# Performance work log

Hardware: AMD Instinct MI355X
Metric: run time of the kernel (lower is better)

## Reference

```python
import jax, jax.numpy as jnp
import numpy as np

NUM_HEADS = 16
ROPE_THETA = 10000.0
SCALE_FACTOR = 1.0  # max_position_embeddings / block_size


def _rope_cos_sin(T, head_dim, dtype):
    # standard RoPE frequencies: inv_freq_i = theta^(-2i/d)
    inv_freq = 1.0 / (ROPE_THETA ** (jnp.arange(0, head_dim, 2, dtype=jnp.float32) / head_dim))
    pos = jnp.arange(T, dtype=jnp.float32) / SCALE_FACTOR
    ang = pos[:, None] * inv_freq[None, :]            # (T, D/2)
    ang = jnp.concatenate([ang, ang], axis=-1)        # (T, D)
    return jnp.cos(ang).astype(dtype)[None, None], jnp.sin(ang).astype(dtype)[None, None]


def _rotate_half(u):
    d = u.shape[-1] // 2
    return jnp.concatenate([-u[..., d:], u[..., :d]], axis=-1)


def setup_inputs() -> dict:
    key = jax.random.key(0)
    ks = jax.random.split(key, 5)
    B, T, C = 2, 2048, 1024
    x = jax.random.normal(ks[0], (B, T, C), dtype=jnp.float32)
    Wqkv = jax.random.normal(ks[1], (C, 3 * C), dtype=jnp.float32) * (1.0 / np.sqrt(C))
    bqkv = jnp.zeros((3 * C,), dtype=jnp.float32)
    Wproj = jax.random.normal(ks[2], (C, C), dtype=jnp.float32) * (1.0 / np.sqrt(C))
    bproj = jnp.zeros((C,), dtype=jnp.float32)
    return {"x": x, "Wqkv": Wqkv, "bqkv": bqkv, "Wproj": Wproj, "bproj": bproj}


def reference(x, Wqkv, bqkv, Wproj, bproj):
    B, T, C = x.shape
    H = NUM_HEADS
    D = C // H
    qkv = x @ Wqkv + bqkv                              # (B, T, 3C)
    q, k, v = jnp.split(qkv, 3, axis=-1)
    # (B, H, T, D)
    q = q.reshape(B, T, H, D).transpose(0, 2, 1, 3)
    k = k.reshape(B, T, H, D).transpose(0, 2, 1, 3)
    v = v.reshape(B, T, H, D).transpose(0, 2, 1, 3)
    cos, sin = _rope_cos_sin(T, D, x.dtype)
    q = q * cos + _rotate_half(q) * sin
    k = k * cos + _rotate_half(k) * sin
    att = jnp.einsum('bhtd,bhsd->bhts', q, k) / jnp.sqrt(jnp.asarray(D, x.dtype))
    causal = jnp.tril(jnp.ones((T, T), dtype=bool))
    att = jnp.where(causal[None, None], att, jnp.asarray(-jnp.inf, att.dtype))
    att = jax.nn.softmax(att, axis=-1)
    y = jnp.einsum('bhts,bhsd->bhtd', att, v)          # (B, H, T, D)
    y = y.transpose(0, 2, 1, 3).reshape(B, T, C)
    return y @ Wproj + bproj
```

## Files before the change

### kernel.cpp

```cpp
#include <hip/hip_runtime.h>
#include <hip/hip_bf16.h>

typedef __hip_bfloat16 bf16;
typedef __attribute__((ext_vector_type(8))) __bf16 bf16x8;
typedef __attribute__((ext_vector_type(4))) __bf16 bf16x4;
typedef __attribute__((ext_vector_type(4))) float f32x4;
typedef unsigned short u16;

#define MFMA16(a, b, c) __builtin_amdgcn_mfma_f32_16x16x32_bf16((a), (b), (c), 0, 0, 0)

static constexpr int B_ = 2, T_ = 2048, C_ = 1024, H_ = 16, D_ = 64;
static constexpr int BT = B_ * T_;
static constexpr int N3 = 3 * C_;

__device__ __forceinline__ void gload16(void* lds, const void* g) {
    __builtin_amdgcn_global_load_lds(
        (const __attribute__((address_space(1))) unsigned int*)g,
        (__attribute__((address_space(3))) unsigned int*)lds, 16, 0, 0);
}

__device__ __forceinline__ u16 bb(float x) {
    return __builtin_bit_cast(u16, __float2bfloat16(x));
}


__global__ void k_transpose_w(const float* __restrict__ src, bf16* __restrict__ dst,
                              int K, int N) {
    __shared__ float t[32][33];
    int bx = blockIdx.x * 32;
    int by = blockIdx.y * 32;
    int tx = threadIdx.x & 31, ty = threadIdx.x >> 5;
#pragma unroll
    for (int i = 0; i < 32; i += 8)
        t[ty + i][tx] = src[(size_t)(by + ty + i) * N + bx + tx];
    __syncthreads();
#pragma unroll
    for (int i = 0; i < 32; i += 8)
        dst[(size_t)(bx + ty + i) * K + by + tx] = __float2bfloat16(t[tx][ty + i]);
}

__global__ void k_convert_x(const float* __restrict__ src, bf16* __restrict__ dst, int n4) {
    int i = blockIdx.x * 256 + threadIdx.x;
    if (i >= n4) return;
    float4 v = reinterpret_cast<const float4*>(src)[i];
    dst[4 * i + 0] = __float2bfloat16(v.x);
    dst[4 * i + 1] = __float2bfloat16(v.y);
    dst[4 * i + 2] = __float2bfloat16(v.z);
    dst[4 * i + 3] = __float2bfloat16(v.w);
}

__global__ void k_rope_table(float* __restrict__ ct, float* __restrict__ st) {
    int i = blockIdx.x * 256 + threadIdx.x;
    if (i >= T_ * 32) return;
    int t = i >> 5, f = i & 31;
    float invf = exp2f(-(float)f * 0.4152410118609203f);
    float ang = (float)t * invf;
    ct[i] = cosf(ang);
    st[i] = sinf(ang);
}

__global__ __launch_bounds__(256) void k_gemm_qkv(
    const bf16* __restrict__ A, const bf16* __restrict__ Bt,
    const float* __restrict__ bias,
    const float* __restrict__ ct, const float* __restrict__ st,
    bf16* __restrict__ q, bf16* __restrict__ kk, bf16* __restrict__ vt) {
    __shared__ bf16 lA[2][128 * 32];
    __shared__ bf16 lB[2][128 * 32];
    const int tid = threadIdx.x;
    const int wave = tid >> 6, lane = tid & 63;
    const int wm = wave >> 1, wn = wave & 1;
    const int l16 = lane & 15, lg = lane >> 4;
    const int m0 = blockIdx.y * 128, n0 = blockIdx.x * 128;

    f32x4 acc[4][4];
#pragma unroll
    for (int i = 0; i < 4; i++)
#pragma unroll
        for (int j = 0; j < 4; j++) acc[i][j] = (f32x4){0.f, 0.f, 0.f, 0.f};

    const int r = lane >> 2;
    const int sc = (lane & 3) ^ (r & 3);
    const bf16* gA = A + (size_t)(m0 + wave * 32 + r) * 1024 + sc * 8;
    const bf16* gB = Bt + (size_t)(n0 + wave * 32 + r) * 1024 + sc * 8;
    const int sw = (lg ^ (l16 & 3)) * 8;

    auto stage = [&](int buf, int k0) {
        bf16* sA = lA[buf] + wave * 1024;
        bf16* sB = lB[buf] + wave * 1024;
        gload16(sA, gA + k0);
        gload16(sA + 512, gA + (size_t)16 * 1024 + k0);
        gload16(sB, gB + k0);
        gload16(sB + 512, gB + (size_t)16 * 1024 + k0);
    };

    stage(0, 0);
    int buf = 0;
    for (int k0 = 0; k0 < 1024; k0 += 32) {
        __syncthreads();
        if (k0 + 32 < 1024) stage(buf ^ 1, k0 + 32);
        bf16x8 af[4], bfr[4];
#pragma unroll
        for (int mi = 0; mi < 4; mi++)
            af[mi] = *(const bf16x8*)(lA[buf] + (wm * 64 + mi * 16 + l16) * 32 + sw);
#pragma unroll
        for (int nj = 0; nj < 4; nj++)
            bfr[nj] = *(const bf16x8*)(lB[buf] + (wn * 64 + nj * 16 + l16) * 32 + sw);
#pragma unroll
        for (int mi = 0; mi < 4; mi++)
#pragma unroll
            for (int nj = 0; nj < 4; nj++)
                acc[mi][nj] = MFMA16(af[mi], bfr[nj], acc[mi][nj]);
        buf ^= 1;
    }

    const int b = m0 >> 11;
#pragma unroll
    for (int mi = 0; mi < 4; mi++) {
        int mbase = m0 + wm * 64 + mi * 16 + lg * 4;
#pragma unroll
        for (int nj = 0; nj < 4; nj++) {
            int n = n0 + wn * 64 + nj * 16 + l16;
            int which = n >> 10;
            int nq = n & 1023;
            int h = nq >> 6, d = nq & 63;
#pragma unroll
            for (int rr = 0; rr < 4; rr++) {
                int m = mbase + rr;
                int t = m & 2047;
                float v = acc[mi][nj][rr] + bias[n];
                if (which == 2) {
                    vt[((size_t)(b * 16 + h) * 64 + d) * 2048 + t] = __float2bfloat16(v);
                } else {
                    float pv = acc[mi][nj ^ 2][rr] + bias[n ^ 32];
                    float c = ct[t * 32 + (d & 31)];
                    float s = st[t * 32 + (d & 31)];
                    float rh = (d < 32) ? -pv : pv;
                    float o = v * c + rh * s;
                    bf16* dst = (which == 0) ? q : kk;
                    dst[((size_t)(b * 16 + h) * 2048 + t) * 64 + d] = __float2bfloat16(o);
                }
            }
        }
    }
}

__global__ __launch_bounds__(256, 4) void k_attn(
    const bf16* __restrict__ qg, const bf16* __restrict__ kg,
    const bf16* __restrict__ vtg, bf16* __restrict__ y) {
    __shared__ bf16 smem[2][2][4096];
    const int wv = threadIdx.x >> 6;
    const int pair = wv >> 1, qh = wv & 1;
    const int lane = threadIdx.x & 63;
    const int l16 = lane & 15, lg = lane >> 4;
    const int id = blockIdx.x;
    const int bh = id & 31;
    const int s = 31 - (id >> 5);
    const int q0w = s * 64 + 32 * qh;
    const bf16* qh_p = qg + (size_t)bh * (2048 * 64);
    const bf16* kh = kg + (size_t)bh * (2048 * 64);
    const bf16* vh = vtg + (size_t)bh * (64 * 2048);

    bf16x8 qf[2][2];
#pragma unroll
    for (int g = 0; g < 2; g++)
#pragma unroll
        for (int h = 0; h < 2; h++)
            qf[g][h] = *(const bf16x8*)(qh_p + (size_t)(q0w + 16 * g + l16) * 64 + 32 * h + 8 * lg);

    f32x4 o[2][4];
#pragma unroll
    for (int g = 0; g < 2; g++)
#pragma unroll
        for (int dt = 0; dt < 4; dt++) o[g][dt] = (f32x4){0.f, 0.f, 0.f, 0.f};
    float mm[2] = {-1e30f, -1e30f}, ls[2] = {0.f, 0.f};

    auto stage = [&](int buf, int kt) {
        bf16* lk = &smem[pair][buf][0];
        bf16* lv = &smem[pair][buf][2048];
#pragma unroll
        for (int i = 0; i < 2; i++) {
            int cc = 2 * qh + i;
            {
                int row = 8 * cc + (lane >> 3);
                int scc = (lane & 7) ^ (lane >> 3);
                gload16(&lk[cc * 512], kh + (size_t)(kt + row) * 64 + scc * 8);
            }
            {
                int row = 16 * cc + (lane >> 2);
                int su = (lane & 3) ^ ((lane >> 3) & 3);
                gload16(&lv[cc * 512], vh + (size_t)row * 2048 + kt + su * 8);
            }
        }
    };

    const f32x4 z = (f32x4){0.f, 0.f, 0.f, 0.f};
    auto compute = [&](int buf, bool diag) {
        const bf16* lk = &smem[pair][buf][0];
        const bf16* lv = &smem[pair][buf][2048];
        bf16x8 kf2[2][2];
#pragma unroll
        for (int t = 0; t < 2; t++)
#pragma unroll
            for (int h = 0; h < 2; h++) {
                int krow = 16 * t + l16;
                int koff = ((h * 64 + lg * 16) ^ ((l16 & 7) << 4)) >> 1;
                kf2[t][h] = *(const bf16x8*)(&lk[krow * 64 + koff]);
            }
        bf16x8 vf[4];
#pragma unroll
        for (int dt = 0; dt < 4; dt++) {
            int vrow = 16 * dt + l16;
            int rs = (l16 >> 1) & 3;
            const bf16* vb = &lv[vrow * 32];
            bf16x4 lo = *(const bf16x4*)(vb + (((lg >> 1) ^ rs) * 8 + (lg & 1) * 4));
            bf16x4 hi = *(const bf16x4*)(vb + (((2 + (lg >> 1)) ^ rs) * 8 + (lg & 1) * 4));
            vf[dt] = __builtin_shufflevector(lo, hi, 0, 1, 2, 3, 4, 5, 6, 7);
        }
        f32x4 sg[2][2];
#pragma unroll
        for (int g = 0; g < 2; g++)
#pragma unroll
            for (int t = 0; t < 2; t++) {
                f32x4 acc = MFMA16(kf2[t][0], qf[g][0], z);
                sg[g][t] = MFMA16(kf2[t][1], qf[g][1], acc);
            }
#pragma unroll
        for (int g = 0; g < 2; g++) {
            float p[8];
#pragma unroll
            for (int t = 0; t < 2; t++)
#pragma unroll
                for (int rr = 0; rr < 4; rr++) {
                    float v = sg[g][t][rr] * 0.125f;
                    if (diag && (16 * t + 4 * lg + rr > 16 * g + l16)) v = -1e30f;
                    p[4 * t + rr] = v;
                }
            float pm = p[0];
#pragma unroll
            for (int i = 1; i < 8; i++) pm = fmaxf(pm, p[i]);
            pm = fmaxf(pm, __shfl_xor(pm, 16, 64));
            pm = fmaxf(pm, __shfl_xor(pm, 32, 64));
            float mn = fmaxf(mm[g], pm);
            float al = __expf(mm[g] - mn);
#pragma unroll
            for (int dt = 0; dt < 4; dt++) o[g][dt] *= al;
            ls[g] *= al;
            mm[g] = mn;
            float ps = 0.f;
#pragma unroll
            for (int i = 0; i < 8; i++) {
                p[i] = __expf(p[i] - mn);
                ps += p[i];
            }
            ls[g] += ps;
            bf16x8 pf;
#pragma unroll
            for (int j = 0; j < 8; j++)
                pf[j] = __builtin_bit_cast(__bf16, __float2bfloat16(p[j]));
#pragma unroll
            for (int dt = 0; dt < 4; dt++) o[g][dt] = MFMA16(vf[dt], pf, o[g][dt]);
        }
    };

    const int base = pair ? (s + 1) : 0;
    const int niter = s + 1;
    stage(0, 32 * base);
    for (int i = 0; i < niter; ++i) {
        __syncthreads();
        if (i + 1 < niter) stage((i + 1) & 1, 32 * (base + i + 1));
        int kt = 32 * (base + i);
        if (kt <= q0w) compute(i & 1, kt == q0w);
    }

    __syncthreads();
    float* mg = (float*)&smem[0][0][0];
    if (pair == 1) {
        float* pp = mg + (qh * 64 + lane) * 36;
        pp[0] = mm[0]; pp[1] = mm[1]; pp[2] = ls[0]; pp[3] = ls[1];
#pragma unroll
        for (int g = 0; g < 2; g++)
#pragma unroll
            for (int dt = 0; dt < 4; dt++)
#pragma unroll
                for (int rr = 0; rr < 4; rr++)
                    pp[4 + g * 16 + dt * 4 + rr] = o[g][dt][rr];
    }
    __syncthreads();
    if (pair == 0) {
        const float* pp = mg + (qh * 64 + lane) * 36;
#pragma unroll
        for (int g = 0; g < 2; g++) {
            float m1 = pp[g], l1 = pp[2 + g];
            float mn = fmaxf(mm[g], m1);
            float a0 = __expf(mm[g] - mn);
            float a1 = __expf(m1 - mn);
            ls[g] = ls[g] * a0 + l1 * a1;
#pragma unroll
            for (int dt = 0; dt < 4; dt++)
#pragma unroll
                for (int rr = 0; rr < 4; rr++)
                    o[g][dt][rr] = o[g][dt][rr] * a0 + pp[4 + g * 16 + dt * 4 + rr] * a1;
        }
        const int b = bh >> 4, h = bh & 15;
#pragma unroll
        for (int g = 0; g < 2; g++) {
            float lt = ls[g];
            lt += __shfl_xor(lt, 16, 64);
            lt += __shfl_xor(lt, 32, 64);
            float inv = 1.f / lt;
            bf16* yp = y + ((size_t)(b * 2048 + q0w + 16 * g + l16)) * 1024 + h * 64 + 4 * lg;
#pragma unroll
            for (int dt = 0; dt < 4; dt++) {
                *(ushort4*)(yp + 16 * dt) = make_ushort4(
                    bb(o[g][dt][0] * inv), bb(o[g][dt][1] * inv),
                    bb(o[g][dt][2] * inv), bb(o[g][dt][3] * inv));
            }
        }
    }
}

__global__ __launch_bounds__(256) void k_gemm_proj(
    const bf16* __restrict__ A, const bf16* __restrict__ Bt,
    const float* __restrict__ bias, float* __restrict__ out) {
    __shared__ bf16 lA[2][128 * 32];
    __shared__ bf16 lB[2][128 * 32];
    const int tid = threadIdx.x;
    const int wave = tid >> 6, lane = tid & 63;
    const int wm = wave >> 1, wn = wave & 1;
    const int l16 = lane & 15, lg = lane >> 4;
    const int m0 = blockIdx.y * 128, n0 = blockIdx.x * 128;

    f32x4 acc[4][4];
#pragma unroll
    for (int i = 0; i < 4; i++)
#pragma unroll
        for (int j = 0; j < 4; j++) acc[i][j] = (f32x4){0.f, 0.f, 0.f, 0.f};

    const int r = lane >> 2;
    const int sc = (lane & 3) ^ (r & 3);
    const bf16* gA = A + (size_t)(m0 + wave * 32 + r) * 1024 + sc * 8;
    const bf16* gB = Bt + (size_t)(n0 + wave * 32 + r) * 1024 + sc * 8;
    const int sw = (lg ^ (l16 & 3)) * 8;

    auto stage = [&](int buf, int k0) {
        bf16* sA = lA[buf] + wave * 1024;
        bf16* sB = lB[buf] + wave * 1024;
        gload16(sA, gA + k0);
        gload16(sA + 512, gA + (size_t)16 * 1024 + k0);
        gload16(sB, gB + k0);
        gload16(sB + 512, gB + (size_t)16 * 1024 + k0);
    };

    stage(0, 0);
    int buf = 0;
    for (int k0 = 0; k0 < 1024; k0 += 32) {
        __syncthreads();
        if (k0 + 32 < 1024) stage(buf ^ 1, k0 + 32);
        bf16x8 af[4], bfr[4];
#pragma unroll
        for (int mi = 0; mi < 4; mi++)
            af[mi] = *(const bf16x8*)(lA[buf] + (wm * 64 + mi * 16 + l16) * 32 + sw);
#pragma unroll
        for (int nj = 0; nj < 4; nj++)
            bfr[nj] = *(const bf16x8*)(lB[buf] + (wn * 64 + nj * 16 + l16) * 32 + sw);
#pragma unroll
        for (int mi = 0; mi < 4; mi++)
#pragma unroll
            for (int nj = 0; nj < 4; nj++)
                acc[mi][nj] = MFMA16(af[mi], bfr[nj], acc[mi][nj]);
        buf ^= 1;
    }

#pragma unroll
    for (int mi = 0; mi < 4; mi++) {
        int mbase = m0 + wm * 64 + mi * 16 + lg * 4;
#pragma unroll
        for (int nj = 0; nj < 4; nj++) {
            int n = n0 + wn * 64 + nj * 16 + l16;
#pragma unroll
            for (int rr = 0; rr < 4; rr++) {
                out[(size_t)(mbase + rr) * 1024 + n] = acc[mi][nj][rr] + bias[n];
            }
        }
    }
}

extern "C" void kernel_launch(void* const* d_in, const int* in_sizes, int n_in,
                              void* d_out, int out_size, void* d_ws, size_t ws_size,
                              hipStream_t stream) {
    const float* x = (const float*)d_in[0];
    const float* Wqkv = (const float*)d_in[1];
    const float* bqkv = (const float*)d_in[2];
    const float* Wproj = (const float*)d_in[3];
    const float* bproj = (const float*)d_in[4];
    float* out = (float*)d_out;

    char* ws = (char*)d_ws;
    bf16* xb = (bf16*)ws;      ws += (size_t)BT * C_ * 2;
    bf16* wqkvT = (bf16*)ws;   ws += (size_t)N3 * C_ * 2;
    bf16* wprojT = (bf16*)ws;  ws += (size_t)C_ * C_ * 2;
    bf16* qb = (bf16*)ws;      ws += (size_t)B_ * H_ * T_ * D_ * 2;
    bf16* kb = (bf16*)ws;      ws += (size_t)B_ * H_ * T_ * D_ * 2;
    bf16* vtb = (bf16*)ws;     ws += (size_t)B_ * H_ * T_ * D_ * 2;
    bf16* yb = (bf16*)ws;      ws += (size_t)BT * C_ * 2;
    float* ct = (float*)ws;    ws += (size_t)T_ * 32 * 4;
    float* st = (float*)ws;    ws += (size_t)T_ * 32 * 4;

    hipLaunchKernelGGL(k_transpose_w, dim3(N3 / 32, C_ / 32), dim3(256), 0, stream,
                       Wqkv, wqkvT, C_, N3);
    hipLaunchKernelGGL(k_transpose_w, dim3(C_ / 32, C_ / 32), dim3(256), 0, stream,
                       Wproj, wprojT, C_, C_);
    hipLaunchKernelGGL(k_convert_x, dim3((BT * C_ / 4) / 256), dim3(256), 0, stream,
                       x, xb, BT * C_ / 4);
    hipLaunchKernelGGL(k_rope_table, dim3((T_ * 32) / 256), dim3(256), 0, stream, ct, st);
    hipLaunchKernelGGL(k_gemm_qkv, dim3(N3 / 128, BT / 128), dim3(256), 0, stream,
                       xb, wqkvT, bqkv, ct, st, qb, kb, vtb);
    hipLaunchKernelGGL(k_attn, dim3(32 * 32), dim3(256), 0, stream,
                       qb, kb, vtb, yb);
    hipLaunchKernelGGL(k_gemm_proj, dim3(C_ / 128, BT / 128), dim3(256), 0, stream,
                       yb, wprojT, bproj, out);
}
```

Measured before the change: 130.9 us.

## Triple-buffer GEMM LDS staging with partial vmcnt waits; raise MFMA priority in attention

Both GEMM kernels move from double to triple-buffered LDS staging. Each iteration waits only until at most the newest stage's loads are outstanding (s_waitcnt vmcnt(4)) plus a raw barrier, rather than a full __syncthreads, so global-to-LDS loads run two tiles ahead of the MFMA compute. The attention kernel wraps its QK and PV MFMA blocks in s_setprio(1) so a wave issuing matrix ops gets scheduling priority over waves doing softmax. Triple buffering raises LDS use per block from 32KB to 48KB, which may reduce occupancy, and correctness depends on the hand-counted vmcnt matching the four loads per stage.

```diff
diff --git a/kernel.cpp b/kernel.cpp
--- a/kernel.cpp
+++ b/kernel.cpp
@@ -64,8 +64,8 @@
     const float* __restrict__ bias,
     const float* __restrict__ ct, const float* __restrict__ st,
     bf16* __restrict__ q, bf16* __restrict__ kk, bf16* __restrict__ vt) {
-    __shared__ bf16 lA[2][128 * 32];
-    __shared__ bf16 lB[2][128 * 32];
+    __shared__ bf16 lA[3][128 * 32];
+    __shared__ bf16 lB[3][128 * 32];
     const int tid = threadIdx.x;
     const int wave = tid >> 6, lane = tid & 63;
     const int wm = wave >> 1, wn = wave & 1;
@@ -92,12 +92,7 @@
         gload16(sB, gB + k0);
         gload16(sB + 512, gB + (size_t)16 * 1024 + k0);
     };
-
-    stage(0, 0);
-    int buf = 0;
-    for (int k0 = 0; k0 < 1024; k0 += 32) {
-        __syncthreads();
-        if (k0 + 32 < 1024) stage(buf ^ 1, k0 + 32);
+    auto compute = [&](int buf) {
         bf16x8 af[4], bfr[4];
 #pragma unroll
         for (int mi = 0; mi < 4; mi++)
@@ -110,8 +105,26 @@
 #pragma unroll
             for (int nj = 0; nj < 4; nj++)
                 acc[mi][nj] = MFMA16(af[mi], bfr[nj], acc[mi][nj]);
-        buf ^= 1;
-    }
+    };
+
+    stage(0, 0);
+    stage(1, 32);
+    int buf = 0;
+    for (int k0 = 0; k0 < 992; k0 += 32) {
+        asm volatile("s_waitcnt vmcnt(4)" ::: "memory");
+        __builtin_amdgcn_s_barrier();
+        __builtin_amdgcn_sched_barrier(0);
+        if (k0 + 64 < 1024) {
+            int nb = buf + 2; if (nb >= 3) nb -= 3;
+            stage(nb, k0 + 64);
+        }
+        compute(buf);
+        buf = (buf == 2) ? 0 : buf + 1;
+    }
+    asm volatile("s_waitcnt vmcnt(0)" ::: "memory");
+    __builtin_amdgcn_s_barrier();
+    __builtin_amdgcn_sched_barrier(0);
+    compute(buf);
 
     const int b = m0 >> 11;
 #pragma unroll
@@ -217,6 +230,7 @@
             vf[dt] = __builtin_shufflevector(lo, hi, 0, 1, 2, 3, 4, 5, 6, 7);
         }
         f32x4 sg[2][2];
+        __builtin_amdgcn_s_setprio(1);
 #pragma unroll
         for (int g = 0; g < 2; g++)
 #pragma unroll
@@ -224,6 +238,7 @@
                 f32x4 acc = MFMA16(kf2[t][0], qf[g][0], z);
                 sg[g][t] = MFMA16(kf2[t][1], qf[g][1], acc);
             }
+        __builtin_amdgcn_s_setprio(0);
 #pragma unroll
         for (int g = 0; g < 2; g++) {
             float p[8];
@@ -257,8 +272,10 @@
 #pragma unroll
             for (int j = 0; j < 8; j++)
                 pf[j] = __builtin_bit_cast(__bf16, __float2bfloat16(p[j]));
+            __builtin_amdgcn_s_setprio(1);
 #pragma unroll
             for (int dt = 0; dt < 4; dt++) o[g][dt] = MFMA16(vf[dt], pf, o[g][dt]);
+            __builtin_amdgcn_s_setprio(0);
         }
     };
 
@@ -322,8 +339,8 @@
 __global__ __launch_bounds__(256) void k_gemm_proj(
     const bf16* __restrict__ A, const bf16* __restrict__ Bt,
     const float* __restrict__ bias, float* __restrict__ out) {
-    __shared__ bf16 lA[2][128 * 32];
-    __shared__ bf16 lB[2][128 * 32];
+    __shared__ bf16 lA[3][128 * 32];
+    __shared__ bf16 lB[3][128 * 32];
     const int tid = threadIdx.x;
     const int wave = tid >> 6, lane = tid & 63;
     const int wm = wave >> 1, wn = wave & 1;
@@ -350,12 +367,7 @@
         gload16(sB, gB + k0);
         gload16(sB + 512, gB + (size_t)16 * 1024 + k0);
     };
-
-    stage(0, 0);
-    int buf = 0;
-    for (int k0 = 0; k0 < 1024; k0 += 32) {
-        __syncthreads();
-        if (k0 + 32 < 1024) stage(buf ^ 1, k0 + 32);
+    auto compute = [&](int buf) {
         bf16x8 af[4], bfr[4];
 #pragma unroll
         for (int mi = 0; mi < 4; mi++)
@@ -368,8 +380,26 @@
 #pragma unroll
             for (int nj = 0; nj < 4; nj++)
                 acc[mi][nj] = MFMA16(af[mi], bfr[nj], acc[mi][nj]);
-        buf ^= 1;
-    }
+    };
+
+    stage(0, 0);
+    stage(1, 32);
+    int buf = 0;
+    for (int k0 = 0; k0 < 992; k0 += 32) {
+        asm volatile("s_waitcnt vmcnt(4)" ::: "memory");
+        __builtin_amdgcn_s_barrier();
+        __builtin_amdgcn_sched_barrier(0);
+        if (k0 + 64 < 1024) {
+            int nb = buf + 2; if (nb >= 3) nb -= 3;
+            stage(nb, k0 + 64);
+        }
+        compute(buf);
+        buf = (buf == 2) ? 0 : buf + 1;
+    }
+    asm volatile("s_waitcnt vmcnt(0)" ::: "memory");
+    __builtin_amdgcn_s_barrier();
+    __builtin_amdgcn_sched_barrier(0);
+    compute(buf);
 
 #pragma unroll
     for (int mi = 0; mi < 4; mi++) {
```

Result: slower. 133.8 us (+2.2%).
